# Optimization experiments

Measured on AMD Instinct MI355X. Metric: run time of the kernel, lower is better.

Reference implementation:

```python
import jax, jax.numpy as jnp
import numpy as np

N_NODES = 100000


def setup_inputs() -> dict:
    key = jax.random.key(0)
    k1, k2, k3, k4 = jax.random.split(key, 4)
    E = 1600000
    D_IN, D_OUT = 256, 256
    feat = jax.random.normal(k1, (N_NODES, D_IN), dtype=jnp.float32)
    src = jax.random.randint(k2, (E,), 0, N_NODES, dtype=jnp.int32)
    dst = jax.random.randint(k3, (E,), 0, N_NODES, dtype=jnp.int32)
    # xavier_uniform-like init for weight
    limit = np.sqrt(6.0 / (D_IN + D_OUT)).astype(np.float32)
    weight = jax.random.uniform(k4, (D_IN, D_OUT), dtype=jnp.float32,
                                minval=-limit, maxval=limit)
    bias = jnp.zeros((D_OUT,), dtype=jnp.float32)
    return {"feat": feat, "src": src, "dst": dst, "weight": weight, "bias": bias}


def reference(feat, src, dst, weight, bias):
    ones = jnp.ones(src.shape[0], dtype=feat.dtype)
    # out_degrees: number of outgoing edges per node (src counts)
    out_deg = jax.ops.segment_sum(ones, src, num_segments=N_NODES)
    # in_degrees: number of incoming edges per node (dst counts)
    in_deg = jax.ops.segment_sum(ones, dst, num_segments=N_NODES)
    # norm == 'both': pre-scale by out_deg^-0.5
    pre = jnp.power(jnp.clip(out_deg, 1.0), -0.5)[:, None]  # [N,1]
    h = feat * pre
    # message passing: copy_src + sum over incoming edges (SpMM)
    agg = jax.ops.segment_sum(h[src], dst, num_segments=N_NODES)  # [N, D_in]
    # dense projection
    rst = agg @ weight  # [N, D_out]
    # post-scale by in_deg^-0.5
    post = jnp.power(jnp.clip(in_deg, 1.0), -0.5)[:, None]
    rst = rst * post + bias
    return rst
```

## Files before the change

### kernel.cpp

```cpp
#include <hip/hip_runtime.h>
#include <hip/hip_bf16.h>
#include <stdint.h>


using short8  = __attribute__((ext_vector_type(8))) short;
using floatx4 = __attribute__((ext_vector_type(4))) float;
using ushort8 = __attribute__((ext_vector_type(8))) unsigned short;

static __device__ __forceinline__ unsigned short f32_to_bf16(float f) {
    unsigned int u = __float_as_uint(f);
    u += 0x7FFFu + ((u >> 16) & 1u);
    return (unsigned short)(u >> 16);
}
static __device__ __forceinline__ float bf2f(unsigned short u) {
    return __uint_as_float((unsigned int)u << 16);
}

__global__ void k_deg(const int* __restrict__ src, const int* __restrict__ dst,
                      int E, int* __restrict__ outc, int* __restrict__ inc) {
    int i = blockIdx.x * blockDim.x + threadIdx.x;
    if (i < E) {
        atomicAdd(&outc[src[i]], 1);
        atomicAdd(&inc[dst[i]], 1);
    }
}

__global__ void k_off(const int* __restrict__ inc, int N, int* __restrict__ total,
                      int* __restrict__ cursor) {
    __shared__ int ss[256];
    __shared__ int sbase;
    int t = threadIdx.x;
    int i = blockIdx.x * 256 + t;
    int d = (i < N) ? inc[i] : 0;
    int v = d;
    ss[t] = v;
    __syncthreads();
    for (int off = 1; off < 256; off <<= 1) {
        int u = (t >= off) ? ss[t - off] : 0;
        __syncthreads();
        v += u;
        ss[t] = v;
        __syncthreads();
    }
    if (t == 255) sbase = atomicAdd(total, v);
    __syncthreads();
    if (i < N) cursor[i] = sbase + (v - d);
}

__global__ void k_fill(const int* __restrict__ src, const int* __restrict__ dst,
                       int E, int* __restrict__ cursor, int* __restrict__ eidx) {
    int i = blockIdx.x * blockDim.x + threadIdx.x;
    if (i < E) {
        int p = atomicAdd(&cursor[dst[i]], 1);
        eidx[p] = src[i];
    }
}

__global__ void k_wt(const float* __restrict__ W, unsigned short* __restrict__ WT) {
    int i = blockIdx.x * blockDim.x + threadIdx.x;
    int n = i >> 8, k = i & 255;
    WT[n * 256 + k] = f32_to_bf16(W[(size_t)k * 256 + n]);
}

__global__ void __launch_bounds__(256)
k_gemm(const float* __restrict__ feat, const int* __restrict__ outc,
       const unsigned short* __restrict__ WT, int N,
       unsigned short* __restrict__ z) {
    int wave = blockIdx.x * 4 + (threadIdx.x >> 6);
    int m0 = wave * 16;
    if (m0 >= N) return;
    int lane = threadIdx.x & 63;
    int r = lane & 15;
    int g = lane >> 4;

    int row = m0 + r;
    float p = rsqrtf((float)max(outc[row], 1));
    const float4* arow = (const float4*)(feat + (size_t)row * 256);

    floatx4 acc[16];
#pragma unroll
    for (int n = 0; n < 16; ++n) acc[n] = (floatx4){0.f, 0.f, 0.f, 0.f};

#pragma unroll
    for (int k = 0; k < 8; ++k) {
        float4 v0 = arow[k * 8 + g * 2];
        float4 v1 = arow[k * 8 + g * 2 + 1];
        short8 a;
        a[0] = (short)f32_to_bf16(v0.x * p);
        a[1] = (short)f32_to_bf16(v0.y * p);
        a[2] = (short)f32_to_bf16(v0.z * p);
        a[3] = (short)f32_to_bf16(v0.w * p);
        a[4] = (short)f32_to_bf16(v1.x * p);
        a[5] = (short)f32_to_bf16(v1.y * p);
        a[6] = (short)f32_to_bf16(v1.z * p);
        a[7] = (short)f32_to_bf16(v1.w * p);
#pragma unroll
        for (int n = 0; n < 16; ++n) {
            short8 b = *(const short8*)(WT + (size_t)(n * 16 + r) * 256 + k * 32 + g * 8);
            acc[n] = __builtin_amdgcn_mfma_f32_16x16x32_bf16(a, b, acc[n], 0, 0, 0);
        }
    }

#pragma unroll
    for (int n = 0; n < 16; ++n) {
        int c = n * 16 + r;
#pragma unroll
        for (int i = 0; i < 4; ++i) {
            int rw = m0 + g * 4 + i;
            z[(size_t)rw * 256 + c] = f32_to_bf16(acc[n][i]);
        }
    }
}

__global__ void k_agg(const unsigned short* __restrict__ z,
                      const int* __restrict__ cursor, const int* __restrict__ inc,
                      const int* __restrict__ eidx, const float* __restrict__ bias,
                      int N, float* __restrict__ out) {
    int node = blockIdx.x * 4 + (threadIdx.x >> 6);
    if (node >= N) return;
    int lane = threadIdx.x & 63;
    int half = lane >> 5;
    int l = lane & 31;
    int deg = inc[node];
    const int* ep = eidx + (cursor[node] - deg);

    float acc[8];
#pragma unroll
    for (int j = 0; j < 8; ++j) acc[j] = 0.f;

    int e = 0;
    for (; e + 1 < deg; e += 2) {
        int s = ep[e + half];
        ushort8 v = *(const ushort8*)(z + (size_t)s * 256 + l * 8);
#pragma unroll
        for (int j = 0; j < 8; ++j) acc[j] += bf2f(v[j]);
    }
    if (e < deg && half == 0) {
        int s = ep[e];
        ushort8 v = *(const ushort8*)(z + (size_t)s * 256 + l * 8);
#pragma unroll
        for (int j = 0; j < 8; ++j) acc[j] += bf2f(v[j]);
    }
#pragma unroll
    for (int j = 0; j < 8; ++j) acc[j] += __shfl_xor(acc[j], 32);

    float post = rsqrtf((float)max(deg, 1));
    int c0 = l * 8 + half * 4;
    float4 bs = *(const float4*)(bias + c0);
    float4 o;
    o.x = acc[half * 4 + 0] * post + bs.x;
    o.y = acc[half * 4 + 1] * post + bs.y;
    o.z = acc[half * 4 + 2] * post + bs.z;
    o.w = acc[half * 4 + 3] * post + bs.w;
    *(float4*)(out + (size_t)node * 256 + c0) = o;
}

extern "C" void kernel_launch(void* const* d_in, const int* in_sizes, int n_in,
                              void* d_out, int out_size, void* d_ws, size_t ws_size,
                              hipStream_t stream) {
    const float* feat = (const float*)d_in[0];
    const int*   src  = (const int*)d_in[1];
    const int*   dst  = (const int*)d_in[2];
    const float* W    = (const float*)d_in[3];
    const float* bias = (const float*)d_in[4];
    float* out = (float*)d_out;

    const int D = 256;
    int N = in_sizes[0] / D;
    int E = in_sizes[1];

    char* ws = (char*)d_ws;
    size_t off = 0;
    auto alloc = [&](size_t bytes) -> void* {
        void* p = ws + off;
        off += (bytes + 255) & ~(size_t)255;
        return p;
    };
    int*            cnt    = (int*)alloc(((size_t)2 * N + 64) * sizeof(int));
    int*            outc   = cnt;
    int*            inc    = cnt + N;
    int*            total  = cnt + 2 * N;
    int*            cursor = (int*)alloc((size_t)N * sizeof(int));
    int*            eidx   = (int*)alloc((size_t)E * sizeof(int));
    unsigned short* z      = (unsigned short*)alloc((size_t)N * D * sizeof(unsigned short));
    unsigned short* WT     = (unsigned short*)alloc((size_t)D * D * sizeof(unsigned short));
    (void)ws_size;

    hipMemsetAsync(cnt, 0, ((size_t)2 * N + 64) * sizeof(int), stream);

    k_deg <<<(E + 255) / 256, 256, 0, stream>>>(src, dst, E, outc, inc);
    k_off <<<(N + 255) / 256, 256, 0, stream>>>(inc, N, total, cursor);
    k_fill<<<(E + 255) / 256, 256, 0, stream>>>(src, dst, E, cursor, eidx);
    k_wt  <<<(D * D) / 256, 256, 0, stream>>>(W, WT);
    k_gemm<<<(N / 16 + 3) / 4, 256, 0, stream>>>(feat, outc, WT, N, z);
    k_agg <<<(N + 3) / 4, 256, 0, stream>>>(z, cursor, inc, eidx, bias, N, out);
}
```

Baseline: 653.4 us.

## Stage W tiles in swizzled LDS for GEMM and permute z column layout

The GEMM kernel now uses 512-thread blocks of 8 waves that cooperatively load half of the bf16 transposed weight into a 64KB XOR-swizzled LDS buffer per K-half. The MFMA B operands are then read from LDS instead of each wave re-reading WT from global memory or cache. Output z rows are written in a permuted column order as two 16-byte vector stores instead of scattered 2-byte stores. The aggregation kernel undoes that permutation with scalar column-scattered stores, trading its float4 output writes for coalesced z writes. The LDS use limits occupancy, and the scalar output stores in aggregation may cost bandwidth.

```diff
diff --git a/kernel.cpp b/kernel.cpp
--- a/kernel.cpp
+++ b/kernel.cpp
@@ -62,52 +62,75 @@
     WT[n * 256 + k] = f32_to_bf16(W[(size_t)k * 256 + n]);
 }
 
-__global__ void __launch_bounds__(256)
+__global__ void __launch_bounds__(512, 4)
 k_gemm(const float* __restrict__ feat, const int* __restrict__ outc,
        const unsigned short* __restrict__ WT, int N,
        unsigned short* __restrict__ z) {
-    int wave = blockIdx.x * 4 + (threadIdx.x >> 6);
-    int m0 = wave * 16;
-    if (m0 >= N) return;
-    int lane = threadIdx.x & 63;
-    int r = lane & 15;
-    int g = lane >> 4;
-
-    int row = m0 + r;
-    float p = rsqrtf((float)max(outc[row], 1));
-    const float4* arow = (const float4*)(feat + (size_t)row * 256);
+    __shared__ unsigned short ldsB[256 * 128];
+
+    int tid  = threadIdx.x;
+    int wave = tid >> 6;
+    int lane = tid & 63;
+    int rl   = lane & 15;
+    int g    = lane >> 4;
+    int wm0  = blockIdx.x * 128 + wave * 16;
+    int rowc = min(wm0 + rl, N - 1);
+    float p  = rsqrtf((float)max(outc[rowc], 1));
+    const float4* arow = (const float4*)(feat + (size_t)rowc * 256);
+    int smask = (rl & 7) << 4;
 
     floatx4 acc[16];
 #pragma unroll
     for (int n = 0; n < 16; ++n) acc[n] = (floatx4){0.f, 0.f, 0.f, 0.f};
 
 #pragma unroll
-    for (int k = 0; k < 8; ++k) {
-        float4 v0 = arow[k * 8 + g * 2];
-        float4 v1 = arow[k * 8 + g * 2 + 1];
-        short8 a;
-        a[0] = (short)f32_to_bf16(v0.x * p);
-        a[1] = (short)f32_to_bf16(v0.y * p);
-        a[2] = (short)f32_to_bf16(v0.z * p);
-        a[3] = (short)f32_to_bf16(v0.w * p);
-        a[4] = (short)f32_to_bf16(v1.x * p);
-        a[5] = (short)f32_to_bf16(v1.y * p);
-        a[6] = (short)f32_to_bf16(v1.z * p);
-        a[7] = (short)f32_to_bf16(v1.w * p);
-#pragma unroll
-        for (int n = 0; n < 16; ++n) {
-            short8 b = *(const short8*)(WT + (size_t)(n * 16 + r) * 256 + k * 32 + g * 8);
-            acc[n] = __builtin_amdgcn_mfma_f32_16x16x32_bf16(a, b, acc[n], 0, 0, 0);
+    for (int h = 0; h < 2; ++h) {
+        if (h) __syncthreads();
+#pragma unroll
+        for (int i = 0; i < 8; ++i) {
+            int c    = i * 512 + tid;
+            int r2   = c >> 4;
+            int colb = (c & 15) << 4;
+            ushort8 v = *(const ushort8*)(WT + r2 * 256 + h * 128 + (colb >> 1));
+            int dst = r2 * 128 + ((colb ^ ((r2 & 7) << 4)) >> 1);
+            *(ushort8*)(&ldsB[dst]) = v;
         }
-    }
-
-#pragma unroll
-    for (int n = 0; n < 16; ++n) {
-        int c = n * 16 + r;
-#pragma unroll
-        for (int i = 0; i < 4; ++i) {
-            int rw = m0 + g * 4 + i;
-            z[(size_t)rw * 256 + c] = f32_to_bf16(acc[n][i]);
+        __syncthreads();
+
+#pragma unroll
+        for (int k2 = 0; k2 < 4; ++k2) {
+            float4 v0 = arow[h * 32 + k2 * 8 + g * 2];
+            float4 v1 = arow[h * 32 + k2 * 8 + g * 2 + 1];
+            short8 a;
+            a[0] = (short)f32_to_bf16(v0.x * p);
+            a[1] = (short)f32_to_bf16(v0.y * p);
+            a[2] = (short)f32_to_bf16(v0.z * p);
+            a[3] = (short)f32_to_bf16(v0.w * p);
+            a[4] = (short)f32_to_bf16(v1.x * p);
+            a[5] = (short)f32_to_bf16(v1.y * p);
+            a[6] = (short)f32_to_bf16(v1.z * p);
+            a[7] = (short)f32_to_bf16(v1.w * p);
+            int cb = (k2 * 64 + g * 16) ^ smask;
+#pragma unroll
+            for (int n = 0; n < 16; ++n) {
+                short8 b = *(const short8*)(&ldsB[(n * 16 + rl) * 128 + (cb >> 1)]);
+                acc[n] = __builtin_amdgcn_mfma_f32_16x16x32_bf16(a, b, acc[n], 0, 0, 0);
+            }
+        }
+    }
+
+#pragma unroll
+    for (int i = 0; i < 4; ++i) {
+        int rw = wm0 + g * 4 + i;
+        if (rw < N) {
+            ushort8 u0, u1;
+#pragma unroll
+            for (int j = 0; j < 8; ++j) {
+                u0[j] = f32_to_bf16(acc[j][i]);
+                u1[j] = f32_to_bf16(acc[8 + j][i]);
+            }
+            *(ushort8*)(z + (size_t)rw * 256 + rl * 16)     = u0;
+            *(ushort8*)(z + (size_t)rw * 256 + rl * 16 + 8) = u1;
         }
     }
 }
@@ -145,14 +168,12 @@
     for (int j = 0; j < 8; ++j) acc[j] += __shfl_xor(acc[j], 32);
 
     float post = rsqrtf((float)max(deg, 1));
-    int c0 = l * 8 + half * 4;
-    float4 bs = *(const float4*)(bias + c0);
-    float4 o;
-    o.x = acc[half * 4 + 0] * post + bs.x;
-    o.y = acc[half * 4 + 1] * post + bs.y;
-    o.z = acc[half * 4 + 2] * post + bs.z;
-    o.w = acc[half * 4 + 3] * post + bs.w;
-    *(float4*)(out + (size_t)node * 256 + c0) = o;
+#pragma unroll
+    for (int jj = 0; jj < 4; ++jj) {
+        int pcol = l * 8 + half * 4 + jj;
+        int c = ((pcol & 15) << 4) | (pcol >> 4);
+        out[(size_t)node * 256 + c] = acc[half * 4 + jj] * post + bias[c];
+    }
 }
 
 extern "C" void kernel_launch(void* const* d_in, const int* in_sizes, int n_in,
@@ -192,6 +213,6 @@
     k_off <<<(N + 255) / 256, 256, 0, stream>>>(inc, N, total, cursor);
     k_fill<<<(E + 255) / 256, 256, 0, stream>>>(src, dst, E, cursor, eidx);
     k_wt  <<<(D * D) / 256, 256, 0, stream>>>(W, WT);
-    k_gemm<<<(N / 16 + 3) / 4, 256, 0, stream>>>(feat, outc, WT, N, z);
+    k_gemm<<<(N + 127) / 128, 512, 0, stream>>>(feat, outc, WT, N, z);
     k_agg <<<(N + 3) / 4, 256, 0, stream>>>(z, cursor, inc, eidx, bias, N, out);
 }
```

Measured after the change: 566.8 us. 13.2% less time.
